# Kernel tuning notes

Hardware: AMD Instinct MI355X
Metric: run time of the kernel (lower is better)

The kernel has to match this reference:

```python
import jax, jax.numpy as jnp
import numpy as np
import math

DT = 1024
HID = 512
B, M, N = 16, 1024, 1024
NEG_INF = -1.0e9


def _linear(x, w, b):
    # torch nn.Linear convention: w is (out, in)
    return x @ w.T + b


def setup_inputs() -> dict:
    key = jax.random.key(0)
    ks = jax.random.split(key, 20)
    s = 0.02
    inp = {
        "oV": jax.random.normal(ks[0], (B, M, DT), jnp.float32),
        "oT": jax.random.normal(ks[1], (B, N, DT), jnp.float32),
        "Wq_v_w": jax.random.normal(ks[2], (DT, DT), jnp.float32) * s,
        "Wq_v_b": jnp.zeros((DT,), jnp.float32),
        "Wk_t_w": jax.random.normal(ks[3], (DT, DT), jnp.float32) * s,
        "Wk_t_b": jnp.zeros((DT,), jnp.float32),
        "Wv_t_w": jax.random.normal(ks[4], (DT, DT), jnp.float32) * s,
        "Wv_t_b": jnp.zeros((DT,), jnp.float32),
        "Wq_t_w": jax.random.normal(ks[5], (DT, DT), jnp.float32) * s,
        "Wq_t_b": jnp.zeros((DT,), jnp.float32),
        "Wk_v_w": jax.random.normal(ks[6], (DT, DT), jnp.float32) * s,
        "Wk_v_b": jnp.zeros((DT,), jnp.float32),
        "Wv_v_w": jax.random.normal(ks[7], (DT, DT), jnp.float32) * s,
        "Wv_v_b": jnp.zeros((DT,), jnp.float32),
        "ffn1_w": jax.random.normal(ks[8], (HID, 2 * DT), jnp.float32) * s,
        "ffn1_b": jnp.zeros((HID,), jnp.float32),
        "ffn2_w": jax.random.normal(ks[9], (1, HID), jnp.float32) * s,
        "ffn2_b": jnp.zeros((1,), jnp.float32),
    }
    return inp


def reference(oV, oT, Wq_v_w, Wq_v_b, Wk_t_w, Wk_t_b, Wv_t_w, Wv_t_b,
              Wq_t_w, Wq_t_b, Wk_v_w, Wk_v_b, Wv_v_w, Wv_v_b,
              ffn1_w, ffn1_b, ffn2_w, ffn2_b):
    dt = oV.shape[-1]
    inv_sqrt = 1.0 / math.sqrt(dt)

    # shared similarity-derived mask
    sim_raw = jnp.einsum('bmd,bnd->bmn', oV, oT)            # (B, m, n)
    v_pool = oV.mean(axis=1)                                  # (B, dt)
    t_pool = oT.mean(axis=1)                                  # (B, dt)
    h = jax.nn.relu(_linear(jnp.concatenate([v_pool, t_pool], axis=-1), ffn1_w, ffn1_b))
    l = jax.nn.sigmoid(_linear(h, ffn2_w, ffn2_b))[:, 0]      # (B,)
    S = jax.nn.softmax(sim_raw * inv_sqrt, axis=-1)
    Mmask = S >= l[:, None, None]                             # (B, m, n) bool

    # V -> T masked cross-attention
    Q_v = _linear(oV, Wq_v_w, Wq_v_b)
    K_t = _linear(oT, Wk_t_w, Wk_t_b)
    V_t = _linear(oT, Wv_t_w, Wv_t_b)
    scores_vt = jnp.einsum('bmd,bnd->bmn', Q_v, K_t) * inv_sqrt
    attn_vt = jax.nn.softmax(jnp.where(Mmask, scores_vt, NEG_INF), axis=-1)
    out_vt = jnp.einsum('bmn,bnd->bmd', attn_vt, V_t)

    # T -> V masked cross-attention (transposed mask)
    Q_t = _linear(oT, Wq_t_w, Wq_t_b)
    K_v = _linear(oV, Wk_v_w, Wk_v_b)
    V_v = _linear(oV, Wv_v_w, Wv_v_b)
    scores_tv = jnp.einsum('bnd,bmd->bnm', Q_t, K_v) * inv_sqrt
    attn_tv = jax.nn.softmax(jnp.where(Mmask.transpose(0, 2, 1), scores_tv, NEG_INF), axis=-1)
    out_tv = jnp.einsum('bnm,bmd->bnd', attn_tv, V_v)

    return out_vt, out_tv, Mmask.astype(jnp.float32)
```

## Files before the change

kernel.cpp:

```cpp
#include <hip/hip_runtime.h>
#include <stdint.h>

typedef unsigned short u16;
typedef unsigned char  u8;
typedef unsigned int   u32;
typedef __attribute__((ext_vector_type(8))) short  short8;
typedef __attribute__((ext_vector_type(4))) float  floatx4;

#define Bz   16
#define Mm   1024
#define Nn   1024
#define Dd   1024
#define HIDh 512
#define INV_SQRT_D 0.03125f
#define NEGINF (-1.0e9f)
#define BMDc  ((size_t)Bz * Mm * Dd)
#define sMDc  ((long)Mm * Dd)

__device__ __forceinline__ float bf2f(u16 h) {
    union { u32 u; float f; } c; c.u = ((u32)h) << 16; return c.f;
}
__device__ __forceinline__ u16 f2bf(float f) {
    union { float f; u32 u; } c; c.f = f;
    u32 u = c.u;
    return (u16)((u + 0x7FFFu + ((u >> 16) & 1u)) >> 16);
}
__device__ __forceinline__ void g2lds16(const u16* g, u16* l) {
    __builtin_amdgcn_global_load_lds((const __attribute__((address_space(1))) void*)g,
                                     (__attribute__((address_space(3))) void*)l, 16, 0, 0);
}

__device__ __forceinline__ float waveSum(float v) {
#pragma unroll
    for (int o = 32; o > 0; o >>= 1) v += __shfl_xor(v, o);
    return v;
}
__device__ __forceinline__ float waveMax(float v) {
#pragma unroll
    for (int o = 32; o > 0; o >>= 1) v = fmaxf(v, __shfl_xor(v, o));
    return v;
}

template <bool OUT_FP32, bool BIAS, bool TRANSC>
__global__ __launch_bounds__(512, 2) void gemm256(
    const u16* __restrict__ A, const u16* __restrict__ Bm,
    const float* __restrict__ bias, void* __restrict__ Cv,
    int K, int ldc, long sA, long sB, long sC)
{
    __shared__ __align__(16) u16 lds[2][2][256 * 64];
    const int tid  = threadIdx.x;
    const int lane = tid & 63;
    const int wv   = tid >> 6;
    const int wr   = wv >> 2;
    const int wc   = wv & 3;
    const int fr   = lane & 15, fq = lane >> 4;

    const int gX = gridDim.x, gY = gridDim.y;
    int bid = blockIdx.x + gX * (blockIdx.y + gY * blockIdx.z);
    const int nwg = gX * gY * gridDim.z;
    int wg = (bid & 7) * (nwg >> 3) + (bid >> 3);
    const int bx = wg % gX; wg /= gX;
    const int by = wg % gY;
    const int bz = wg / gY;

    const long tileM = (long)bx * 256, tileN = (long)by * 256;
    A  += (long)bz * sA;
    Bm += (long)bz * sB;
    const int T = K >> 6;

    floatx4 acc[8][4];
#pragma unroll
    for (int i = 0; i < 8; ++i)
#pragma unroll
        for (int j = 0; j < 4; ++j) acc[i][j] = (floatx4){0.f, 0.f, 0.f, 0.f};

    const int lrow = lane >> 3;
    const int scol = ((lane & 7) ^ lrow) << 3;
    const int sw   = fr & 7;
    const int kc0  = ((fq ^ sw) << 3);
    const int kc1  = (((4 + fq) ^ sw) << 3);

    auto stage = [&](int tt, int side, int hh, int bb) {
#pragma unroll
        for (int i = 0; i < 2; ++i) {
            const int j = i * 8 + wv;
            const int prow = side ? (((j >> 2) << 6) + (hh << 5) + ((j & 3) << 3))
                                  : (((j >> 3) << 7) + (hh << 6) + ((j & 7) << 3));
            const u16* src = side ? Bm : A;
            const long rb  = side ? tileN : tileM;
            g2lds16(src + (size_t)(rb + prow + lrow) * (size_t)K + (size_t)(tt << 6) + scol,
                    &lds[bb][side][prow * 64]);
        }
    };

    short8 Af[4][2], Bf[4][2];
    auto quad = [&](int mb, int nb) {
#pragma unroll
        for (int m = 0; m < 4; ++m)
#pragma unroll
            for (int n = 0; n < 2; ++n) {
                acc[mb + m][nb + n] = __builtin_amdgcn_mfma_f32_16x16x32_bf16(
                    Af[m][0], Bf[nb + n][0], acc[mb + m][nb + n], 0, 0, 0);
                acc[mb + m][nb + n] = __builtin_amdgcn_mfma_f32_16x16x32_bf16(
                    Af[m][1], Bf[nb + n][1], acc[mb + m][nb + n], 0, 0, 0);
            }
    };

    stage(0, 0, 0, 0); stage(0, 1, 0, 0); stage(0, 1, 1, 0); stage(0, 0, 1, 0);
    stage(1, 0, 0, 1); stage(1, 1, 1, 1); stage(1, 0, 1, 1);
    asm volatile("s_waitcnt vmcnt(6)" ::: "memory");
    __builtin_amdgcn_s_barrier();

    for (int t = 0; t < T; ++t) {
        const int cb = t & 1;
        const u16* lA = &lds[cb][0][0];
        const u16* lB = &lds[cb][1][0];

#pragma unroll
        for (int m = 0; m < 4; ++m) {
            const int ro = ((wr << 7) + (m << 4) + fr) * 64;
            Af[m][0] = *(const short8*)&lA[ro + kc0];
            Af[m][1] = *(const short8*)&lA[ro + kc1];
        }
#pragma unroll
        for (int n = 0; n < 2; ++n) {
            const int ro = ((wc << 6) + (n << 4) + fr) * 64;
            Bf[n][0] = *(const short8*)&lB[ro + kc0];
            Bf[n][1] = *(const short8*)&lB[ro + kc1];
        }
        if (t + 1 < T) stage(t + 1, 1, 0, cb ^ 1);
        asm volatile("" ::: "memory");
        __builtin_amdgcn_s_barrier();
        asm volatile("s_waitcnt lgkmcnt(0)" ::: "memory");
        __builtin_amdgcn_sched_barrier(0);
        __builtin_amdgcn_s_setprio(1);
        quad(0, 0);
        __builtin_amdgcn_s_setprio(0);
        asm volatile("" ::: "memory");
        __builtin_amdgcn_s_barrier();

#pragma unroll
        for (int n = 2; n < 4; ++n) {
            const int ro = ((wc << 6) + (n << 4) + fr) * 64;
            Bf[n][0] = *(const short8*)&lB[ro + kc0];
            Bf[n][1] = *(const short8*)&lB[ro + kc1];
        }
        if (t + 2 < T) stage(t + 2, 0, 0, cb);
        asm volatile("" ::: "memory");
        __builtin_amdgcn_s_barrier();
        asm volatile("s_waitcnt lgkmcnt(0)" ::: "memory");
        __builtin_amdgcn_sched_barrier(0);
        __builtin_amdgcn_s_setprio(1);
        quad(0, 2);
        __builtin_amdgcn_s_setprio(0);
        asm volatile("" ::: "memory");
        __builtin_amdgcn_s_barrier();

#pragma unroll
        for (int m = 0; m < 4; ++m) {
            const int ro = ((wr << 7) + ((m + 4) << 4) + fr) * 64;
            Af[m][0] = *(const short8*)&lA[ro + kc0];
            Af[m][1] = *(const short8*)&lA[ro + kc1];
        }
        if (t + 2 < T) stage(t + 2, 1, 1, cb);
        asm volatile("" ::: "memory");
        __builtin_amdgcn_s_barrier();
        asm volatile("s_waitcnt lgkmcnt(0)" ::: "memory");
        __builtin_amdgcn_sched_barrier(0);
        __builtin_amdgcn_s_setprio(1);
        quad(4, 2);
        __builtin_amdgcn_s_setprio(0);
        asm volatile("" ::: "memory");
        __builtin_amdgcn_s_barrier();

        if (t + 2 < T) stage(t + 2, 0, 1, cb);
        asm volatile("" ::: "memory");
        __builtin_amdgcn_s_barrier();
        __builtin_amdgcn_s_setprio(1);
        quad(4, 0);
        __builtin_amdgcn_s_setprio(0);
        if (t + 1 < T) {
            if (t + 2 < T) asm volatile("s_waitcnt vmcnt(6)" ::: "memory");
            else           asm volatile("s_waitcnt vmcnt(0)" ::: "memory");
        }
        asm volatile("" ::: "memory");
        __builtin_amdgcn_s_barrier();
    }

#pragma unroll
    for (int j = 0; j < 4; ++j) {
        const long col = tileN + (wc << 6) + (j << 4) + fr;
        float bv = 0.f;
        if constexpr (BIAS) bv = bias[col];
#pragma unroll
        for (int i = 0; i < 8; ++i) {
            const long row0 = tileM + (wr << 7) + (i << 4) + (fq << 2);
#pragma unroll
            for (int r = 0; r < 4; ++r) {
                const float v = acc[i][j][r] + bv;
                const long row = row0 + r;
                if constexpr (OUT_FP32) {
                    ((float*)Cv + (long)bz * sC)[row * ldc + col] = v;
                } else if constexpr (TRANSC) {
                    const long b = row >> 10, mloc = row & 1023;
                    ((u16*)Cv)[b * sMDc + col * Mm + mloc] = f2bf(v);
                } else {
                    ((u16*)Cv + (long)bz * sC)[row * ldc + col] = f2bf(v);
                }
            }
        }
    }
}

__global__ __launch_bounds__(256) void conv_kernel(
    const float* __restrict__ src, u16* __restrict__ dst, size_t n8)
{
    const size_t stride = (size_t)gridDim.x * 256;
    for (size_t i = (size_t)blockIdx.x * 256 + threadIdx.x; i < n8; i += stride) {
        const float4 a = ((const float4*)src)[2 * i];
        const float4 b = ((const float4*)src)[2 * i + 1];
        short8 o;
        o[0]=(short)f2bf(a.x); o[1]=(short)f2bf(a.y); o[2]=(short)f2bf(a.z); o[3]=(short)f2bf(a.w);
        o[4]=(short)f2bf(b.x); o[5]=(short)f2bf(b.y); o[6]=(short)f2bf(b.z); o[7]=(short)f2bf(b.w);
        *(short8*)(dst + 8 * i) = o;
    }
}

__global__ __launch_bounds__(256) void wconv6(
    const float* __restrict__ w0, const float* __restrict__ w1, const float* __restrict__ w2,
    const float* __restrict__ w3, const float* __restrict__ w4, const float* __restrict__ w5,
    u16* __restrict__ dst)
{
    const float* src;
    switch (blockIdx.y) {
        case 0: src = w0; break; case 1: src = w1; break; case 2: src = w2; break;
        case 3: src = w3; break; case 4: src = w4; break; default: src = w5; break;
    }
    const size_t i = (size_t)blockIdx.x * 256 + threadIdx.x;
    const float4 a = ((const float4*)src)[2 * i];
    const float4 b = ((const float4*)src)[2 * i + 1];
    short8 o;
    o[0]=(short)f2bf(a.x); o[1]=(short)f2bf(a.y); o[2]=(short)f2bf(a.z); o[3]=(short)f2bf(a.w);
    o[4]=(short)f2bf(b.x); o[5]=(short)f2bf(b.y); o[6]=(short)f2bf(b.z); o[7]=(short)f2bf(b.w);
    *(short8*)(dst + (((size_t)blockIdx.y) << 20) + 8 * i) = o;
}

__global__ __launch_bounds__(256) void pool_kernel(
    const float* __restrict__ oV, const float* __restrict__ oT,
    float* __restrict__ vpool, float* __restrict__ tpool)
{
    const int col = blockIdx.x * 256 + threadIdx.x;
    const int b = blockIdx.y;
    const int src_i = blockIdx.z & 1, chunk = blockIdx.z >> 1;
    const float* src = (src_i ? oT : oV) + (size_t)b * Mm * Dd;
    const int r0 = chunk * (Mm / 4);
    float s = 0.f;
    for (int r = r0; r < r0 + Mm / 4; ++r) s += src[(size_t)r * Dd + col];
    float* dst = src_i ? tpool : vpool;
    atomicAdd(dst + b * Dd + col, s * (1.0f / Mm));
}

__global__ __launch_bounds__(256) void ffn1_kernel(
    const float* __restrict__ vpool, const float* __restrict__ tpool,
    const float* __restrict__ f1w, const float* __restrict__ f1b,
    float* __restrict__ hbuf)
{
    const int j = blockIdx.x, b = blockIdx.y;
    const int t = threadIdx.x, wv = t >> 6, lane = t & 63;
    __shared__ float red[4];
    const float* w = f1w + (size_t)j * (2 * Dd);
    float a = 0.f;
    for (int k = t; k < Dd; k += 256) a += vpool[b * Dd + k] * w[k];
    for (int k = t; k < Dd; k += 256) a += tpool[b * Dd + k] * w[Dd + k];
    a = waveSum(a);
    if (lane == 0) red[wv] = a;
    __syncthreads();
    if (t == 0) hbuf[b * HIDh + j] = fmaxf(red[0] + red[1] + red[2] + red[3] + f1b[j], 0.0f);
}

__global__ __launch_bounds__(256) void ffn2_kernel(
    const float* __restrict__ hbuf, const float* __restrict__ f2w,
    const float* __restrict__ f2b, float* __restrict__ lbuf)
{
    const int b = blockIdx.x;
    const int t = threadIdx.x, wv = t >> 6, lane = t & 63;
    __shared__ float red[4];
    float p = 0.f;
    for (int j = t; j < HIDh; j += 256) p += hbuf[b * HIDh + j] * f2w[j];
    p = waveSum(p);
    if (lane == 0) red[wv] = p;
    __syncthreads();
    if (t == 0) {
        const float z = red[0] + red[1] + red[2] + red[3] + f2b[0];
        lbuf[b] = 1.0f / (1.0f + expf(-z));
    }
}

__global__ __launch_bounds__(256) void sim_softmax_mask(
    const u16* __restrict__ scores, const float* __restrict__ lbuf, float* __restrict__ maskF)
{
    const int row = blockIdx.x, b = blockIdx.y;
    const int t = threadIdx.x, wv = t >> 6, lane = t & 63;
    __shared__ float red[8];
    const size_t off = ((size_t)b * Mm + row) * Nn;
    const uint2 sv = *(const uint2*)(scores + off + 4 * t);
    const float x0 = bf2f((u16)(sv.x & 0xFFFFu)) * INV_SQRT_D;
    const float x1 = bf2f((u16)(sv.x >> 16))     * INV_SQRT_D;
    const float x2 = bf2f((u16)(sv.y & 0xFFFFu)) * INV_SQRT_D;
    const float x3 = bf2f((u16)(sv.y >> 16))     * INV_SQRT_D;
    float mx = waveMax(fmaxf(fmaxf(x0, x1), fmaxf(x2, x3)));
    if (lane == 0) red[wv] = mx;
    __syncthreads();
    mx = fmaxf(fmaxf(red[0], red[1]), fmaxf(red[2], red[3]));
    const float e0 = expf(x0 - mx), e1 = expf(x1 - mx), e2 = expf(x2 - mx), e3 = expf(x3 - mx);
    float s = waveSum(e0 + e1 + e2 + e3);
    if (lane == 0) red[4 + wv] = s;
    __syncthreads();
    const float inv = 1.0f / fmaxf(red[4] + red[5] + red[6] + red[7], 1e-30f);
    const float l = lbuf[b];
    float4 mk;
    mk.x = (e0 * inv >= l) ? 1.0f : 0.0f;
    mk.y = (e1 * inv >= l) ? 1.0f : 0.0f;
    mk.z = (e2 * inv >= l) ? 1.0f : 0.0f;
    mk.w = (e3 * inv >= l) ? 1.0f : 0.0f;
    *(float4*)(maskF + off + 4 * t) = mk;
}

__global__ __launch_bounds__(256) void transpose_mask(
    const float* __restrict__ maskF, u8* __restrict__ maskT)
{
    __shared__ u8 tile[64][68];
    const int m0 = blockIdx.x * 64, n0 = blockIdx.y * 64, b = blockIdx.z;
    const int t = threadIdx.x;
    const int r = t >> 2, c = (t & 3) * 16;
    const float* src = maskF + ((size_t)b * Mm + (m0 + r)) * Nn + n0 + c;
    float4 f0 = ((const float4*)src)[0];
    float4 f1 = ((const float4*)src)[1];
    float4 f2 = ((const float4*)src)[2];
    float4 f3 = ((const float4*)src)[3];
    u8* dst = &tile[r][c];
    dst[0]=f0.x!=0.f; dst[1]=f0.y!=0.f; dst[2]=f0.z!=0.f; dst[3]=f0.w!=0.f;
    dst[4]=f1.x!=0.f; dst[5]=f1.y!=0.f; dst[6]=f1.z!=0.f; dst[7]=f1.w!=0.f;
    dst[8]=f2.x!=0.f; dst[9]=f2.y!=0.f; dst[10]=f2.z!=0.f; dst[11]=f2.w!=0.f;
    dst[12]=f3.x!=0.f; dst[13]=f3.y!=0.f; dst[14]=f3.z!=0.f; dst[15]=f3.w!=0.f;
    __syncthreads();
    union { u8 b[16]; uint4 v; } pk;
#pragma unroll
    for (int k = 0; k < 16; ++k) pk.b[k] = tile[c + k][r];
    *(uint4*)(maskT + ((size_t)b * Nn + (n0 + r)) * Mm + m0 + c) = pk.v;
}

template <bool TRANSP>
__global__ __launch_bounds__(256) void masked_softmax(
    u16* __restrict__ scores, const float* __restrict__ maskF, const u8* __restrict__ maskT)
{
    const int row = blockIdx.x, b = blockIdx.y;
    const int t = threadIdx.x, wv = t >> 6, lane = t & 63;
    __shared__ float red[8];
    const size_t off = ((size_t)b * Mm + row) * Nn;
    const uint2 sv = *(const uint2*)(scores + off + 4 * t);
    float x0 = bf2f((u16)(sv.x & 0xFFFFu)) * INV_SQRT_D;
    float x1 = bf2f((u16)(sv.x >> 16))     * INV_SQRT_D;
    float x2 = bf2f((u16)(sv.y & 0xFFFFu)) * INV_SQRT_D;
    float x3 = bf2f((u16)(sv.y >> 16))     * INV_SQRT_D;
    if (TRANSP) {
        const u32 mk = *(const u32*)(maskT + off + 4 * t);
        if (!(mk & 0x000000FFu)) x0 = NEGINF;
        if (!(mk & 0x0000FF00u)) x1 = NEGINF;
        if (!(mk & 0x00FF0000u)) x2 = NEGINF;
        if (!(mk & 0xFF000000u)) x3 = NEGINF;
    } else {
        const float4 mk = *(const float4*)(maskF + off + 4 * t);
        if (mk.x == 0.f) x0 = NEGINF;
        if (mk.y == 0.f) x1 = NEGINF;
        if (mk.z == 0.f) x2 = NEGINF;
        if (mk.w == 0.f) x3 = NEGINF;
    }
    float mx = waveMax(fmaxf(fmaxf(x0, x1), fmaxf(x2, x3)));
    if (lane == 0) red[wv] = mx;
    __syncthreads();
    mx = fmaxf(fmaxf(red[0], red[1]), fmaxf(red[2], red[3]));
    const float e0 = expf(x0 - mx), e1 = expf(x1 - mx), e2 = expf(x2 - mx), e3 = expf(x3 - mx);
    float s = waveSum(e0 + e1 + e2 + e3);
    if (lane == 0) red[4 + wv] = s;
    __syncthreads();
    const float inv = 1.0f / fmaxf(red[4] + red[5] + red[6] + red[7], 1e-30f);
    uint2 pk;
    pk.x = (u32)f2bf(e0 * inv) | ((u32)f2bf(e1 * inv) << 16);
    pk.y = (u32)f2bf(e2 * inv) | ((u32)f2bf(e3 * inv) << 16);
    *(uint2*)(scores + off + 4 * t) = pk;
}

extern "C" void kernel_launch(void* const* d_in, const int* in_sizes, int n_in,
                              void* d_out, int out_size, void* d_ws, size_t ws_size,
                              hipStream_t stream)
{
    (void)in_sizes; (void)n_in; (void)out_size; (void)ws_size;
    const float* oV     = (const float*)d_in[0];
    const float* oT     = (const float*)d_in[1];
    const float* Wq_v_w = (const float*)d_in[2];
    const float* Wq_v_b = (const float*)d_in[3];
    const float* Wk_t_w = (const float*)d_in[4];
    const float* Wk_t_b = (const float*)d_in[5];
    const float* Wv_t_w = (const float*)d_in[6];
    const float* Wv_t_b = (const float*)d_in[7];
    const float* Wq_t_w = (const float*)d_in[8];
    const float* Wq_t_b = (const float*)d_in[9];
    const float* Wk_v_w = (const float*)d_in[10];
    const float* Wk_v_b = (const float*)d_in[11];
    const float* Wv_v_w = (const float*)d_in[12];
    const float* Wv_v_b = (const float*)d_in[13];
    const float* f1w    = (const float*)d_in[14];
    const float* f1b    = (const float*)d_in[15];
    const float* f2w    = (const float*)d_in[16];
    const float* f2b    = (const float*)d_in[17];

    float* out_vt = (float*)d_out;
    float* out_tv = out_vt + BMDc;
    float* maskF  = out_vt + 2 * BMDc;

    u16* S0  = (u16*)d_ws;
    u16* S1  = S0 + BMDc;
    u16* S2  = S1 + BMDc;
    u16* S3  = S2 + BMDc;
    u16* oVb = S3 + BMDc;
    u16* oTb = oVb + BMDc;
    u16* Wc  = oTb + BMDc;
    u8*  maskT = (u8*)(Wc + 6 * (1 << 20));
    float* vpool = (float*)(maskT + BMDc);
    float* tpool = vpool + Bz * Dd;
    float* hbuf  = tpool + Bz * Dd;
    float* lbuf  = hbuf + Bz * HIDh;

    const dim3 blk(256), blk512(512);
    const dim3 gBat(Mm / 256, Nn / 256, Bz);
    const dim3 gProj(Bz * Mm / 256, Dd / 256, 1);
    const dim3 gRow(Mm, Bz);
    const dim3 gTrp(Mm / 64, Nn / 64, Bz);
    const long sMD = sMDc, sMN = (long)Mm * Nn;

    conv_kernel<<<dim3(4096), blk, 0, stream>>>(oV, oVb, BMDc / 8);
    conv_kernel<<<dim3(4096), blk, 0, stream>>>(oT, oTb, BMDc / 8);
    wconv6<<<dim3(512, 6), blk, 0, stream>>>(Wq_v_w, Wk_t_w, Wv_t_w, Wq_t_w, Wk_v_w, Wv_v_w, Wc);

    hipMemsetAsync(vpool, 0, 2 * Bz * Dd * sizeof(float), stream);
    pool_kernel<<<dim3(Dd / 256, Bz, 8), blk, 0, stream>>>(oV, oT, vpool, tpool);
    ffn1_kernel<<<dim3(HIDh, Bz), blk, 0, stream>>>(vpool, tpool, f1w, f1b, hbuf);
    ffn2_kernel<<<dim3(Bz), blk, 0, stream>>>(hbuf, f2w, f2b, lbuf);

    gemm256<false,false,false><<<gBat, blk512, 0, stream>>>(oVb, oTb, nullptr, S3, Dd, Nn, sMD, sMD, sMN);
    sim_softmax_mask<<<gRow, blk, 0, stream>>>(S3, lbuf, maskF);
    transpose_mask<<<gTrp, blk, 0, stream>>>(maskF, maskT);

    gemm256<false,true ,false><<<gProj, blk512, 0, stream>>>(oVb, Wc,                Wq_v_b, S0, Dd, Dd, 0, 0, 0);
    gemm256<false,true ,false><<<gProj, blk512, 0, stream>>>(oTb, Wc + (1 << 20),    Wk_t_b, S1, Dd, Dd, 0, 0, 0);
    gemm256<false,true ,true ><<<gProj, blk512, 0, stream>>>(oTb, Wc + 2 * (1 << 20),Wv_t_b, S2, Dd, Dd, 0, 0, 0);
    gemm256<false,false,false><<<gBat, blk512, 0, stream>>>(S0, S1, nullptr, S3, Dd, Nn, sMD, sMD, sMN);
    masked_softmax<false><<<gRow, blk, 0, stream>>>(S3, maskF, maskT);
    gemm256<true ,false,false><<<gBat, blk512, 0, stream>>>(S3, S2, nullptr, out_vt, Nn, Dd, sMN, sMD, sMD);

    gemm256<false,true ,false><<<gProj, blk512, 0, stream>>>(oTb, Wc + 3 * (1 << 20), Wq_t_b, S0, Dd, Dd, 0, 0, 0);
    gemm256<false,true ,false><<<gProj, blk512, 0, stream>>>(oVb, Wc + 4 * (1 << 20), Wk_v_b, S1, Dd, Dd, 0, 0, 0);
    gemm256<false,true ,true ><<<gProj, blk512, 0, stream>>>(oVb, Wc + 5 * (1 << 20), Wv_v_b, S2, Dd, Dd, 0, 0, 0);
    gemm256<false,false,false><<<gBat, blk512, 0, stream>>>(S0, S1, nullptr, S3, Dd, Nn, sMD, sMD, sMN);
    masked_softmax<true><<<gRow, blk, 0, stream>>>(S3, maskF, maskT);
    gemm256<true ,false,false><<<gBat, blk512, 0, stream>>>(S3, S2, nullptr, out_tv, Nn, Dd, sMN, sMD, sMD);
}
```

Measured before the change: 969.7 us.

## Fuse Q/K/V projections per input into one wide GEMM and merge conversion with pooling

The six projection GEMMs become two launches of a new kernel. Each launch multiplies one input (oV or oT) against three concatenated weight matrices and routes the output columns to the Q, K or V buffers, writing V transposed. The weights are reordered and the biases concatenated to match. The fp32-to-bf16 conversion of oV/oT is also fused with the mean-pooling pass so the inputs are read once instead of twice. This costs extra workspace for six projection buffers and uses a larger grid per launch. The pooled result now depends on atomics spread across 16 row-chunks.

```diff
diff --git a/kernel.cpp b/kernel.cpp
--- a/kernel.cpp
+++ b/kernel.cpp
@@ -212,18 +212,193 @@
     }
 }
 
-__global__ __launch_bounds__(256) void conv_kernel(
-    const float* __restrict__ src, u16* __restrict__ dst, size_t n8)
-{
-    const size_t stride = (size_t)gridDim.x * 256;
-    for (size_t i = (size_t)blockIdx.x * 256 + threadIdx.x; i < n8; i += stride) {
-        const float4 a = ((const float4*)src)[2 * i];
-        const float4 b = ((const float4*)src)[2 * i + 1];
-        short8 o;
-        o[0]=(short)f2bf(a.x); o[1]=(short)f2bf(a.y); o[2]=(short)f2bf(a.z); o[3]=(short)f2bf(a.w);
-        o[4]=(short)f2bf(b.x); o[5]=(short)f2bf(b.y); o[6]=(short)f2bf(b.z); o[7]=(short)f2bf(b.w);
-        *(short8*)(dst + 8 * i) = o;
-    }
+__global__ __launch_bounds__(512, 2) void gemm_proj3(
+    const u16* __restrict__ A, const u16* __restrict__ Bm,
+    const float* __restrict__ bcat,
+    u16* __restrict__ Pq, u16* __restrict__ Pk, u16* __restrict__ Pv, int K)
+{
+    __shared__ __align__(16) u16 lds[2][2][256 * 64];
+    const int tid  = threadIdx.x;
+    const int lane = tid & 63;
+    const int wv   = tid >> 6;
+    const int wr   = wv >> 2;
+    const int wc   = wv & 3;
+    const int fr   = lane & 15, fq = lane >> 4;
+
+    const int gX = gridDim.x, gY = gridDim.y;
+    int bid = blockIdx.x + gX * blockIdx.y;
+    const int nwg = gX * gY;
+    int wg = (bid & 7) * (nwg >> 3) + (bid >> 3);
+    const int bx = wg % gX;
+    const int by = wg / gX;
+
+    const long tileM = (long)bx * 256, tileN = (long)by * 256;
+    const int T = K >> 6;
+
+    floatx4 acc[8][4];
+#pragma unroll
+    for (int i = 0; i < 8; ++i)
+#pragma unroll
+        for (int j = 0; j < 4; ++j) acc[i][j] = (floatx4){0.f, 0.f, 0.f, 0.f};
+
+    const int lrow = lane >> 3;
+    const int scol = ((lane & 7) ^ lrow) << 3;
+    const int sw   = fr & 7;
+    const int kc0  = ((fq ^ sw) << 3);
+    const int kc1  = (((4 + fq) ^ sw) << 3);
+
+    auto stage = [&](int tt, int side, int hh, int bb) {
+#pragma unroll
+        for (int i = 0; i < 2; ++i) {
+            const int j = i * 8 + wv;
+            const int prow = side ? (((j >> 2) << 6) + (hh << 5) + ((j & 3) << 3))
+                                  : (((j >> 3) << 7) + (hh << 6) + ((j & 7) << 3));
+            const u16* src = side ? Bm : A;
+            const long rb  = side ? tileN : tileM;
+            g2lds16(src + (size_t)(rb + prow + lrow) * (size_t)K + (size_t)(tt << 6) + scol,
+                    &lds[bb][side][prow * 64]);
+        }
+    };
+
+    short8 Af[4][2], Bf[4][2];
+    auto quad = [&](int mb, int nb) {
+#pragma unroll
+        for (int m = 0; m < 4; ++m)
+#pragma unroll
+            for (int n = 0; n < 2; ++n) {
+                acc[mb + m][nb + n] = __builtin_amdgcn_mfma_f32_16x16x32_bf16(
+                    Af[m][0], Bf[nb + n][0], acc[mb + m][nb + n], 0, 0, 0);
+                acc[mb + m][nb + n] = __builtin_amdgcn_mfma_f32_16x16x32_bf16(
+                    Af[m][1], Bf[nb + n][1], acc[mb + m][nb + n], 0, 0, 0);
+            }
+    };
+
+    stage(0, 0, 0, 0); stage(0, 1, 0, 0); stage(0, 1, 1, 0); stage(0, 0, 1, 0);
+    stage(1, 0, 0, 1); stage(1, 1, 1, 1); stage(1, 0, 1, 1);
+    asm volatile("s_waitcnt vmcnt(6)" ::: "memory");
+    __builtin_amdgcn_s_barrier();
+
+    for (int t = 0; t < T; ++t) {
+        const int cb = t & 1;
+        const u16* lA = &lds[cb][0][0];
+        const u16* lB = &lds[cb][1][0];
+
+#pragma unroll
+        for (int m = 0; m < 4; ++m) {
+            const int ro = ((wr << 7) + (m << 4) + fr) * 64;
+            Af[m][0] = *(const short8*)&lA[ro + kc0];
+            Af[m][1] = *(const short8*)&lA[ro + kc1];
+        }
+#pragma unroll
+        for (int n = 0; n < 2; ++n) {
+            const int ro = ((wc << 6) + (n << 4) + fr) * 64;
+            Bf[n][0] = *(const short8*)&lB[ro + kc0];
+            Bf[n][1] = *(const short8*)&lB[ro + kc1];
+        }
+        if (t + 1 < T) stage(t + 1, 1, 0, cb ^ 1);
+        asm volatile("" ::: "memory");
+        __builtin_amdgcn_s_barrier();
+        asm volatile("s_waitcnt lgkmcnt(0)" ::: "memory");
+        __builtin_amdgcn_sched_barrier(0);
+        __builtin_amdgcn_s_setprio(1);
+        quad(0, 0);
+        __builtin_amdgcn_s_setprio(0);
+        asm volatile("" ::: "memory");
+        __builtin_amdgcn_s_barrier();
+
+#pragma unroll
+        for (int n = 2; n < 4; ++n) {
+            const int ro = ((wc << 6) + (n << 4) + fr) * 64;
+            Bf[n][0] = *(const short8*)&lB[ro + kc0];
+            Bf[n][1] = *(const short8*)&lB[ro + kc1];
+        }
+        if (t + 2 < T) stage(t + 2, 0, 0, cb);
+        asm volatile("" ::: "memory");
+        __builtin_amdgcn_s_barrier();
+        asm volatile("s_waitcnt lgkmcnt(0)" ::: "memory");
+        __builtin_amdgcn_sched_barrier(0);
+        __builtin_amdgcn_s_setprio(1);
+        quad(0, 2);
+        __builtin_amdgcn_s_setprio(0);
+        asm volatile("" ::: "memory");
+        __builtin_amdgcn_s_barrier();
+
+#pragma unroll
+        for (int m = 0; m < 4; ++m) {
+            const int ro = ((wr << 7) + ((m + 4) << 4) + fr) * 64;
+            Af[m][0] = *(const short8*)&lA[ro + kc0];
+            Af[m][1] = *(const short8*)&lA[ro + kc1];
+        }
+        if (t + 2 < T) stage(t + 2, 1, 1, cb);
+        asm volatile("" ::: "memory");
+        __builtin_amdgcn_s_barrier();
+        asm volatile("s_waitcnt lgkmcnt(0)" ::: "memory");
+        __builtin_amdgcn_sched_barrier(0);
+        __builtin_amdgcn_s_setprio(1);
+        quad(4, 2);
+        __builtin_amdgcn_s_setprio(0);
+        asm volatile("" ::: "memory");
+        __builtin_amdgcn_s_barrier();
+
+        if (t + 2 < T) stage(t + 2, 0, 1, cb);
+        asm volatile("" ::: "memory");
+        __builtin_amdgcn_s_barrier();
+        __builtin_amdgcn_s_setprio(1);
+        quad(4, 0);
+        __builtin_amdgcn_s_setprio(0);
+        if (t + 1 < T) {
+            if (t + 2 < T) asm volatile("s_waitcnt vmcnt(6)" ::: "memory");
+            else           asm volatile("s_waitcnt vmcnt(0)" ::: "memory");
+        }
+        asm volatile("" ::: "memory");
+        __builtin_amdgcn_s_barrier();
+    }
+
+#pragma unroll
+    for (int j = 0; j < 4; ++j) {
+        const long colL = tileN + (wc << 6) + (j << 4) + fr;
+        const int oid = (int)(colL >> 10);
+        const long col = colL & 1023;
+        const float bv = bcat[colL];
+#pragma unroll
+        for (int i = 0; i < 8; ++i) {
+            const long row0 = tileM + (wr << 7) + (i << 4) + (fq << 2);
+#pragma unroll
+            for (int r = 0; r < 4; ++r) {
+                const float v = acc[i][j][r] + bv;
+                const long row = row0 + r;
+                if (oid == 0)      Pq[row * Dd + col] = f2bf(v);
+                else if (oid == 1) Pk[row * Dd + col] = f2bf(v);
+                else { const long b = row >> 10, mloc = row & 1023;
+                       Pv[b * sMDc + col * Mm + mloc] = f2bf(v); }
+            }
+        }
+    }
+}
+
+__global__ __launch_bounds__(256) void conv_pool(
+    const float* __restrict__ oV, const float* __restrict__ oT,
+    u16* __restrict__ oVb, u16* __restrict__ oTb,
+    float* __restrict__ vpool, float* __restrict__ tpool)
+{
+    const int b = blockIdx.y, srci = blockIdx.z;
+    const float* src = (srci ? oT : oV) + (size_t)b * Mm * Dd;
+    u16* dst = (srci ? oTb : oVb) + (size_t)b * Mm * Dd;
+    const int c4 = threadIdx.x * 4;
+    const int r0 = blockIdx.x * 64;
+    float4 s = {0.f, 0.f, 0.f, 0.f};
+    for (int r = r0; r < r0 + 64; ++r) {
+        const float4 v = *(const float4*)&src[(size_t)r * Dd + c4];
+        s.x += v.x; s.y += v.y; s.z += v.z; s.w += v.w;
+        ushort4 o;
+        o.x = f2bf(v.x); o.y = f2bf(v.y); o.z = f2bf(v.z); o.w = f2bf(v.w);
+        *(ushort4*)&dst[(size_t)r * Dd + c4] = o;
+    }
+    float* pool = (srci ? tpool : vpool) + (size_t)b * Dd + c4;
+    atomicAdd(pool + 0, s.x * (1.0f / Mm));
+    atomicAdd(pool + 1, s.y * (1.0f / Mm));
+    atomicAdd(pool + 2, s.z * (1.0f / Mm));
+    atomicAdd(pool + 3, s.w * (1.0f / Mm));
 }
 
 __global__ __launch_bounds__(256) void wconv6(
@@ -245,19 +420,19 @@
     *(short8*)(dst + (((size_t)blockIdx.y) << 20) + 8 * i) = o;
 }
 
-__global__ __launch_bounds__(256) void pool_kernel(
-    const float* __restrict__ oV, const float* __restrict__ oT,
-    float* __restrict__ vpool, float* __restrict__ tpool)
-{
-    const int col = blockIdx.x * 256 + threadIdx.x;
-    const int b = blockIdx.y;
-    const int src_i = blockIdx.z & 1, chunk = blockIdx.z >> 1;
-    const float* src = (src_i ? oT : oV) + (size_t)b * Mm * Dd;
-    const int r0 = chunk * (Mm / 4);
-    float s = 0.f;
-    for (int r = r0; r < r0 + Mm / 4; ++r) s += src[(size_t)r * Dd + col];
-    float* dst = src_i ? tpool : vpool;
-    atomicAdd(dst + b * Dd + col, s * (1.0f / Mm));
+__global__ __launch_bounds__(256) void bcat_kernel(
+    const float* __restrict__ b0, const float* __restrict__ b1, const float* __restrict__ b2,
+    const float* __restrict__ b3, const float* __restrict__ b4, const float* __restrict__ b5,
+    float* __restrict__ out)
+{
+    const int i = blockIdx.x * 256 + threadIdx.x;
+    const int seg = i >> 10;
+    const float* s;
+    switch (seg) {
+        case 0: s = b0; break; case 1: s = b1; break; case 2: s = b2; break;
+        case 3: s = b3; break; case 4: s = b4; break; default: s = b5; break;
+    }
+    out[i] = s[i & 1023];
 }
 
 __global__ __launch_bounds__(256) void ffn1_kernel(
@@ -419,32 +594,35 @@
     float* out_tv = out_vt + BMDc;
     float* maskF  = out_vt + 2 * BMDc;
 
-    u16* S0  = (u16*)d_ws;
-    u16* S1  = S0 + BMDc;
-    u16* S2  = S1 + BMDc;
-    u16* S3  = S2 + BMDc;
+    u16* S0a = (u16*)d_ws;
+    u16* S1a = S0a + BMDc;
+    u16* S2a = S1a + BMDc;
+    u16* S0b = S2a + BMDc;
+    u16* S1b = S0b + BMDc;
+    u16* S2b = S1b + BMDc;
+    u16* S3  = S2b + BMDc;
     u16* oVb = S3 + BMDc;
     u16* oTb = oVb + BMDc;
     u16* Wc  = oTb + BMDc;
     u8*  maskT = (u8*)(Wc + 6 * (1 << 20));
-    float* vpool = (float*)(maskT + BMDc);
+    float* bcat  = (float*)(maskT + BMDc);
+    float* vpool = bcat + 6144;
     float* tpool = vpool + Bz * Dd;
     float* hbuf  = tpool + Bz * Dd;
     float* lbuf  = hbuf + Bz * HIDh;
 
     const dim3 blk(256), blk512(512);
     const dim3 gBat(Mm / 256, Nn / 256, Bz);
-    const dim3 gProj(Bz * Mm / 256, Dd / 256, 1);
+    const dim3 gFproj(Bz * Mm / 256, 3 * Dd / 256, 1);
     const dim3 gRow(Mm, Bz);
     const dim3 gTrp(Mm / 64, Nn / 64, Bz);
     const long sMD = sMDc, sMN = (long)Mm * Nn;
 
-    conv_kernel<<<dim3(4096), blk, 0, stream>>>(oV, oVb, BMDc / 8);
-    conv_kernel<<<dim3(4096), blk, 0, stream>>>(oT, oTb, BMDc / 8);
-    wconv6<<<dim3(512, 6), blk, 0, stream>>>(Wq_v_w, Wk_t_w, Wv_t_w, Wq_t_w, Wk_v_w, Wv_v_w, Wc);
+    wconv6<<<dim3(512, 6), blk, 0, stream>>>(Wq_v_w, Wk_v_w, Wv_v_w, Wq_t_w, Wk_t_w, Wv_t_w, Wc);
+    bcat_kernel<<<dim3(24), blk, 0, stream>>>(Wq_v_b, Wk_v_b, Wv_v_b, Wq_t_b, Wk_t_b, Wv_t_b, bcat);
 
     hipMemsetAsync(vpool, 0, 2 * Bz * Dd * sizeof(float), stream);
-    pool_kernel<<<dim3(Dd / 256, Bz, 8), blk, 0, stream>>>(oV, oT, vpool, tpool);
+    conv_pool<<<dim3(16, Bz, 2), blk, 0, stream>>>(oV, oT, oVb, oTb, vpool, tpool);
     ffn1_kernel<<<dim3(HIDh, Bz), blk, 0, stream>>>(vpool, tpool, f1w, f1b, hbuf);
     ffn2_kernel<<<dim3(Bz), blk, 0, stream>>>(hbuf, f2w, f2b, lbuf);
 
@@ -452,17 +630,14 @@
     sim_softmax_mask<<<gRow, blk, 0, stream>>>(S3, lbuf, maskF);
     transpose_mask<<<gTrp, blk, 0, stream>>>(maskF, maskT);
 
-    gemm256<false,true ,false><<<gProj, blk512, 0, stream>>>(oVb, Wc,                Wq_v_b, S0, Dd, Dd, 0, 0, 0);
-    gemm256<false,true ,false><<<gProj, blk512, 0, stream>>>(oTb, Wc + (1 << 20),    Wk_t_b, S1, Dd, Dd, 0, 0, 0);
-    gemm256<false,true ,true ><<<gProj, blk512, 0, stream>>>(oTb, Wc + 2 * (1 << 20),Wv_t_b, S2, Dd, Dd, 0, 0, 0);
-    gemm256<false,false,false><<<gBat, blk512, 0, stream>>>(S0, S1, nullptr, S3, Dd, Nn, sMD, sMD, sMN);
+    gemm_proj3<<<gFproj, blk512, 0, stream>>>(oVb, Wc,                bcat,        S0a, S1b, S2b, Dd);
+    gemm_proj3<<<gFproj, blk512, 0, stream>>>(oTb, Wc + 3 * (1 << 20), bcat + 3072, S0b, S1a, S2a, Dd);
+
+    gemm256<false,false,false><<<gBat, blk512, 0, stream>>>(S0a, S1a, nullptr, S3, Dd, Nn, sMD, sMD, sMN);
     masked_softmax<false><<<gRow, blk, 0, stream>>>(S3, maskF, maskT);
-    gemm256<true ,false,false><<<gBat, blk512, 0, stream>>>(S3, S2, nullptr, out_vt, Nn, Dd, sMN, sMD, sMD);
-
-    gemm256<false,true ,false><<<gProj, blk512, 0, stream>>>(oTb, Wc + 3 * (1 << 20), Wq_t_b, S0, Dd, Dd, 0, 0, 0);
-    gemm256<false,true ,false><<<gProj, blk512, 0, stream>>>(oVb, Wc + 4 * (1 << 20), Wk_v_b, S1, Dd, Dd, 0, 0, 0);
-    gemm256<false,true ,true ><<<gProj, blk512, 0, stream>>>(oVb, Wc + 5 * (1 << 20), Wv_v_b, S2, Dd, Dd, 0, 0, 0);
-    gemm256<false,false,false><<<gBat, blk512, 0, stream>>>(S0, S1, nullptr, S3, Dd, Nn, sMD, sMD, sMN);
+    gemm256<true ,false,false><<<gBat, blk512, 0, stream>>>(S3, S2a, nullptr, out_vt, Nn, Dd, sMN, sMD, sMD);
+
+    gemm256<false,false,false><<<gBat, blk512, 0, stream>>>(S0b, S1b, nullptr, S3, Dd, Nn, sMD, sMD, sMN);
     masked_softmax<true><<<gRow, blk, 0, stream>>>(S3, maskF, maskT);
-    gemm256<true ,false,false><<<gBat, blk512, 0, stream>>>(S3, S2, nullptr, out_tv, Nn, Dd, sMN, sMD, sMD);
-}
+    gemm256<true ,false,false><<<gBat, blk512, 0, stream>>>(S3, S2b, nullptr, out_tv, Nn, Dd, sMN, sMD, sMD);
+}
```

Measured after the change: 1.011 ms. 1.04x slower.
